# Optimization experiments

Measured on AMD Instinct MI355X. Metric: run time of the kernel, lower is better.

The kernel has to match this reference:

```python
import jax, jax.numpy as jnp
import numpy as np

ALPHA = 0.9          # alpha_mem
THRESHOLD = 1.0
WINDOW = 1.0         # module-level `window`; spike fn receives threshold*window
MEM_SUBTRACT = THRESHOLD  # membrane_subtract defaults to threshold


@jax.custom_vjp
def spike(v):
    # sinabs ThresholdSubtract forward: multiple spikes per step via floor division
    return jnp.where(v > 0, jnp.floor(v / THRESHOLD), 0.0)

def _spike_fwd(v):
    return spike(v), v

def _spike_bwd(v, g):
    # surrogate gradient: boxcar heaviside(v - (threshold - window)) / threshold
    grad = (v >= (THRESHOLD - THRESHOLD * WINDOW)).astype(g.dtype) / THRESHOLD
    return (g * grad,)

spike.defvjp(_spike_fwd, _spike_bwd)


def setup_inputs() -> dict:
    key = jax.random.key(0)
    k1, k2 = jax.random.split(key, 2)
    B, T, N = 32, 1000, 1024
    input_current = jax.random.normal(k1, (B, T, N), dtype=jnp.float32)
    w_rec = jax.random.normal(k2, (N, N), dtype=jnp.float32) * 0.02  # Linear weight [out, in]
    b_rec = jnp.zeros((N,), dtype=jnp.float32)
    return {"input_current": input_current, "w_rec": w_rec, "b_rec": b_rec}


def reference(input_current, w_rec, b_rec):
    B, T, N = input_current.shape

    def step(carry, x_t):
        state, rec = carry                      # [B, N] each
        total = x_t + rec                       # recurrent feedback added to input
        act = spike(state)                      # spikes from state BEFORE integration (1-step delay)
        state = state - act * MEM_SUBTRACT      # membrane subtract after spiking
        state = state * ALPHA + (1.0 - ALPHA) * total  # leaky integration
        rec = act @ w_rec.T + b_rec             # recurrent GEMM for next step
        return (state, rec), act

    state0 = jnp.zeros((B, N), dtype=input_current.dtype)
    rec0 = jnp.zeros((B, N), dtype=input_current.dtype)
    xs = jnp.swapaxes(input_current, 0, 1)      # [T, B, N]
    _, spikes = jax.lax.scan(step, (state0, rec0), xs)
    return jnp.swapaxes(spikes, 0, 1)           # [B, T, N]
```

## Files before the change

### kernel.cpp

```cpp
#include <hip/hip_runtime.h>
#include <cstdint>
#include <cstddef>

#define B_       32
#define T_       1000
#define N_       1024
#define THREADS_ 256
#define WAVES_   4
#define CHUNK_   8
#define NCHUNK_  (T_ / CHUNK_)

typedef float v4f __attribute__((ext_vector_type(4)));

__device__ __forceinline__ void barrier_lds() {
  __asm__ volatile("s_waitcnt lgkmcnt(0)\n\ts_barrier" ::: "memory");
}

#define ISSUE_CHUNK(buf, base)                                              \
  do {                                                                      \
    _Pragma("unroll")                                                       \
    for (int _k = 0; _k < CHUNK_; ++_k) {                                   \
      const v4f* _p = (const v4f*)((base) + (size_t)_k * N_);               \
      __asm__ volatile("global_load_dwordx4 %0, %1, off"                    \
                       : "=&v"(buf[_k])                                     \
                       : "v"(_p)                                            \
                       : "memory");                                         \
    }                                                                       \
  } while (0)

#define WAITBUF(buf, IMM)                                                   \
  __asm__ volatile("s_waitcnt vmcnt(" #IMM ")"                              \
                   : "+v"(buf[0]), "+v"(buf[1]), "+v"(buf[2]),              \
                     "+v"(buf[3]), "+v"(buf[4]), "+v"(buf[5]),              \
                     "+v"(buf[6]), "+v"(buf[7])                             \
                   :                                                        \
                   : "memory")

__global__ __launch_bounds__(THREADS_, 1)
void lif_main(const float* __restrict__ x, const float* __restrict__ w,
              const float* __restrict__ brec_g, float* __restrict__ out)
{
  const int b    = blockIdx.x;
  const int tid  = threadIdx.x;
  const int lane = tid & 63;
  const int wv   = tid >> 6;
  const int n0   = tid << 2;

  const float* xb   = x   + (size_t)b * T_ * N_ + n0;
  float*       outb = out + (size_t)b * T_ * N_ + n0;

  __shared__ unsigned long long s_cmask[2][WAVES_];
  __shared__ unsigned long long s_mask [2][WAVES_];
  __shared__ v4f                s_val  [2][THREADS_];

  v4f state = (v4f)(0.f);
  v4f rec   = (v4f)(0.f);
  const v4f brec = *(const v4f*)(brec_g + n0);

  auto process = [&](const v4f (&xs)[CHUNK_], int c) {
    v4f st = state;
    v4f r  = rec;
    v4f cmax = st;
#pragma unroll
    for (int k = 0; k < CHUNK_; ++k) {
      cmax.x = fmaxf(cmax.x, st.x);
      cmax.y = fmaxf(cmax.y, st.y);
      cmax.z = fmaxf(cmax.z, st.z);
      cmax.w = fmaxf(cmax.w, st.w);
      v4f t = xs[k] + r;
      st = st * 0.9f + 0.1f * t;
      r = brec;
    }
    float m = fmaxf(fmaxf(cmax.x, cmax.y), fmaxf(cmax.z, cmax.w));
    int any = (m >= 1.0f);

    const int p = c & 1;
    unsigned long long wm = __ballot(any);
    if (lane == 0) s_cmask[p][wv] = wm;
    barrier_lds();
    unsigned long long anyblk =
        s_cmask[p][0] | s_cmask[p][1] | s_cmask[p][2] | s_cmask[p][3];

    if (anyblk == 0ULL) {
      state = st;
      rec   = brec;
      return;
    }

    st = state;
    r  = rec;
#pragma unroll 1
    for (int k = 0; k < CHUNK_; ++k) {
      const int q = k & 1;
      float tx = xs[k].x + r.x, ty = xs[k].y + r.y,
            tz = xs[k].z + r.z, tw = xs[k].w + r.w;
      float ax = (st.x > 0.f) ? floorf(st.x) : 0.f;
      float ay = (st.y > 0.f) ? floorf(st.y) : 0.f;
      float az = (st.z > 0.f) ? floorf(st.z) : 0.f;
      float aw = (st.w > 0.f) ? floorf(st.w) : 0.f;
      int ms = (ax != 0.f) | (ay != 0.f) | (az != 0.f) | (aw != 0.f);
      if (ms) {
        v4f v; v.x = ax; v.y = ay; v.z = az; v.w = aw;
        s_val[q][tid] = v;
        size_t ot = (size_t)(c * CHUNK_ + k) * N_;
        if (ax != 0.f) outb[ot + 0] = ax;
        if (ay != 0.f) outb[ot + 1] = ay;
        if (az != 0.f) outb[ot + 2] = az;
        if (aw != 0.f) outb[ot + 3] = aw;
      }
      unsigned long long sm = __ballot(ms);
      if (lane == 0) s_mask[q][wv] = sm;
      st.x = (st.x - ax) * 0.9f + 0.1f * tx;
      st.y = (st.y - ay) * 0.9f + 0.1f * ty;
      st.z = (st.z - az) * 0.9f + 0.1f * tz;
      st.w = (st.w - aw) * 0.9f + 0.1f * tw;
      barrier_lds();
      v4f racc = brec;
#pragma unroll 1
      for (int w2 = 0; w2 < WAVES_; ++w2) {
        unsigned long long mm = s_mask[q][w2];
        while (mm) {
          int l = __builtin_ctzll(mm);
          mm &= mm - 1;
          int j = (w2 << 6) + l;
          v4f v = s_val[q][j];
          int jn = j << 2;
          if (v.x != 0.f) {
            racc.x += v.x * w[(size_t)(n0 + 0) * N_ + jn];
            racc.y += v.x * w[(size_t)(n0 + 1) * N_ + jn];
            racc.z += v.x * w[(size_t)(n0 + 2) * N_ + jn];
            racc.w += v.x * w[(size_t)(n0 + 3) * N_ + jn];
          }
          if (v.y != 0.f) {
            int j1 = jn + 1;
            racc.x += v.y * w[(size_t)(n0 + 0) * N_ + j1];
            racc.y += v.y * w[(size_t)(n0 + 1) * N_ + j1];
            racc.z += v.y * w[(size_t)(n0 + 2) * N_ + j1];
            racc.w += v.y * w[(size_t)(n0 + 3) * N_ + j1];
          }
          if (v.z != 0.f) {
            int j2 = jn + 2;
            racc.x += v.z * w[(size_t)(n0 + 0) * N_ + j2];
            racc.y += v.z * w[(size_t)(n0 + 1) * N_ + j2];
            racc.z += v.z * w[(size_t)(n0 + 2) * N_ + j2];
            racc.w += v.z * w[(size_t)(n0 + 3) * N_ + j2];
          }
          if (v.w != 0.f) {
            int j3 = jn + 3;
            racc.x += v.w * w[(size_t)(n0 + 0) * N_ + j3];
            racc.y += v.w * w[(size_t)(n0 + 1) * N_ + j3];
            racc.z += v.w * w[(size_t)(n0 + 2) * N_ + j3];
            racc.w += v.w * w[(size_t)(n0 + 3) * N_ + j3];
          }
        }
      }
      r = racc;
    }
    state = st;
    rec   = r;
  };

  v4f bufA[CHUNK_], bufB[CHUNK_], bufC[CHUNK_];
  ISSUE_CHUNK(bufA, xb);
  ISSUE_CHUNK(bufB, xb + (size_t)CHUNK_ * N_);

  int c = 0;
#pragma unroll 1
  for (int t3 = 0; t3 < 41; ++t3) {
    ISSUE_CHUNK(bufC, xb + (size_t)(c + 2) * CHUNK_ * N_);
    WAITBUF(bufA, 16);
    process(bufA, c); ++c;
    ISSUE_CHUNK(bufA, xb + (size_t)(c + 2) * CHUNK_ * N_);
    WAITBUF(bufB, 16);
    process(bufB, c); ++c;
    ISSUE_CHUNK(bufB, xb + (size_t)(c + 2) * CHUNK_ * N_);
    WAITBUF(bufC, 16);
    process(bufC, c); ++c;
  }
  WAITBUF(bufA, 8);
  process(bufA, 123);
  WAITBUF(bufB, 0);
  process(bufB, 124);
}

extern "C" void kernel_launch(void* const* d_in, const int* in_sizes, int n_in,
                              void* d_out, int out_size, void* d_ws, size_t ws_size,
                              hipStream_t stream) {
  const float* x  = (const float*)d_in[0];
  const float* w  = (const float*)d_in[1];
  const float* br = (const float*)d_in[2];
  float* out = (float*)d_out;

  hipMemsetAsync(out, 0, (size_t)out_size * sizeof(float), stream);

  lif_main<<<B_, THREADS_, 0, stream>>>(x, w, br, out);
}
```

Baseline: 351.4 us.

## Fuse output zeroing into main kernel, stage input via LDS, defer spike scatter

Replaces the separate memset with 2048 extra zeroing blocks launched alongside the 32 recurrent blocks, so clearing the output overlaps the serial time loop. Input chunks are now copied straight into shared memory with global_load_lds instead of into registers. Spikes are no longer written to the output inside the loop; they go into a per-batch workspace list through a shared atomic counter, and a second kernel scatters them afterwards so they cannot race with the zeroing. This relies on the spike count per batch staying under the capacity, otherwise spikes are silently dropped, and it adds a second kernel launch.

```diff
diff --git a/kernel.cpp b/kernel.cpp
--- a/kernel.cpp
+++ b/kernel.cpp
@@ -9,6 +9,7 @@
 #define WAVES_   4
 #define CHUNK_   8
 #define NCHUNK_  (T_ / CHUNK_)
+#define ZBLOCKS_ 2048
 
 typedef float v4f __attribute__((ext_vector_type(4)));
 
@@ -16,48 +17,65 @@
   __asm__ volatile("s_waitcnt lgkmcnt(0)\n\ts_barrier" ::: "memory");
 }
 
-#define ISSUE_CHUNK(buf, base)                                              \
-  do {                                                                      \
-    _Pragma("unroll")                                                       \
-    for (int _k = 0; _k < CHUNK_; ++_k) {                                   \
-      const v4f* _p = (const v4f*)((base) + (size_t)_k * N_);               \
-      __asm__ volatile("global_load_dwordx4 %0, %1, off"                    \
-                       : "=&v"(buf[_k])                                     \
-                       : "v"(_p)                                            \
-                       : "memory");                                         \
-    }                                                                       \
-  } while (0)
-
-#define WAITBUF(buf, IMM)                                                   \
-  __asm__ volatile("s_waitcnt vmcnt(" #IMM ")"                              \
-                   : "+v"(buf[0]), "+v"(buf[1]), "+v"(buf[2]),              \
-                     "+v"(buf[3]), "+v"(buf[4]), "+v"(buf[5]),              \
-                     "+v"(buf[6]), "+v"(buf[7])                             \
-                   :                                                        \
-                   : "memory")
+#define VMWAIT(N) __asm__ volatile("s_waitcnt vmcnt(" #N ")" ::: "memory")
+
+typedef const __attribute__((address_space(1))) void* gas_ptr;
+typedef __attribute__((address_space(3))) void*       las_ptr;
 
 __global__ __launch_bounds__(THREADS_, 1)
-void lif_main(const float* __restrict__ x, const float* __restrict__ w,
-              const float* __restrict__ brec_g, float* __restrict__ out)
+void lif_fused(const float* __restrict__ x, const float* __restrict__ w,
+               const float* __restrict__ brec_g, float* __restrict__ out,
+               unsigned long long* __restrict__ ws_rec,
+               unsigned int* __restrict__ ws_cnt, int cap)
 {
+  if (blockIdx.x >= B_) {
+    const size_t n4 = (size_t)B_ * T_ * N_ / 4;
+    size_t i = (size_t)(blockIdx.x - B_) * THREADS_ + threadIdx.x;
+    const size_t stride = (size_t)(gridDim.x - B_) * THREADS_;
+    v4f* o4 = (v4f*)out;
+    v4f z = (v4f)(0.f);
+    for (; i < n4; i += stride) __builtin_nontemporal_store(z, &o4[i]);
+    return;
+  }
+
   const int b    = blockIdx.x;
   const int tid  = threadIdx.x;
   const int lane = tid & 63;
   const int wv   = tid >> 6;
   const int n0   = tid << 2;
 
-  const float* xb   = x   + (size_t)b * T_ * N_ + n0;
-  float*       outb = out + (size_t)b * T_ * N_ + n0;
-
+  __shared__ float xbuf0[CHUNK_][N_];
+  __shared__ float xbuf1[CHUNK_][N_];
+  __shared__ float xbuf2[CHUNK_][N_];
   __shared__ unsigned long long s_cmask[2][WAVES_];
   __shared__ unsigned long long s_mask [2][WAVES_];
   __shared__ v4f                s_val  [2][THREADS_];
+  __shared__ unsigned int       s_spkcnt;
+
+  if (tid == 0) s_spkcnt = 0;
+
+  const float* xg = x + (size_t)b * T_ * N_ + (wv << 8) + (lane << 2);
 
   v4f state = (v4f)(0.f);
   v4f rec   = (v4f)(0.f);
   const v4f brec = *(const v4f*)(brec_g + n0);
 
-  auto process = [&](const v4f (&xs)[CHUNK_], int c) {
+#define ISSUE_LDS(bufv, c)                                                   \
+  do {                                                                       \
+    const float* _g = xg + (size_t)(c) * (CHUNK_ * N_);                      \
+    _Pragma("unroll")                                                        \
+    for (int _k = 0; _k < CHUNK_; ++_k)                                      \
+      __builtin_amdgcn_global_load_lds((gas_ptr)(_g + (size_t)_k * N_),      \
+                                       (las_ptr)&bufv[_k][wv << 8],          \
+                                       16, 0, 0);                            \
+  } while (0)
+
+  auto process = [&](const float* xrow, int c) {
+    v4f xs[CHUNK_];
+#pragma unroll
+    for (int k = 0; k < CHUNK_; ++k)
+      xs[k] = *(const v4f*)(xrow + (size_t)k * N_ + n0);
+
     v4f st = state;
     v4f r  = rec;
     v4f cmax = st;
@@ -102,11 +120,18 @@
       if (ms) {
         v4f v; v.x = ax; v.y = ay; v.z = az; v.w = aw;
         s_val[q][tid] = v;
-        size_t ot = (size_t)(c * CHUNK_ + k) * N_;
-        if (ax != 0.f) outb[ot + 0] = ax;
-        if (ay != 0.f) outb[ot + 1] = ay;
-        if (az != 0.f) outb[ot + 2] = az;
-        if (aw != 0.f) outb[ot + 3] = aw;
+        unsigned int off = (unsigned int)((c * CHUNK_ + k) * N_ + n0);
+        float av[4] = {ax, ay, az, aw};
+#pragma unroll
+        for (int e = 0; e < 4; ++e) {
+          if (av[e] != 0.f) {
+            unsigned int idx = atomicAdd(&s_spkcnt, 1u);
+            if ((int)idx < cap)
+              ws_rec[(size_t)b * cap + idx] =
+                  ((unsigned long long)(off + e) << 32) |
+                  (unsigned long long)__float_as_uint(av[e]);
+          }
+        }
       }
       unsigned long long sm = __ballot(ms);
       if (lane == 0) s_mask[q][wv] = sm;
@@ -160,27 +185,50 @@
     rec   = r;
   };
 
-  v4f bufA[CHUNK_], bufB[CHUNK_], bufC[CHUNK_];
-  ISSUE_CHUNK(bufA, xb);
-  ISSUE_CHUNK(bufB, xb + (size_t)CHUNK_ * N_);
+  const float* x0row = &xbuf0[0][0];
+  const float* x1row = &xbuf1[0][0];
+  const float* x2row = &xbuf2[0][0];
+
+  ISSUE_LDS(xbuf0, 0);
+  ISSUE_LDS(xbuf1, 1);
 
   int c = 0;
 #pragma unroll 1
   for (int t3 = 0; t3 < 41; ++t3) {
-    ISSUE_CHUNK(bufC, xb + (size_t)(c + 2) * CHUNK_ * N_);
-    WAITBUF(bufA, 16);
-    process(bufA, c); ++c;
-    ISSUE_CHUNK(bufA, xb + (size_t)(c + 2) * CHUNK_ * N_);
-    WAITBUF(bufB, 16);
-    process(bufB, c); ++c;
-    ISSUE_CHUNK(bufB, xb + (size_t)(c + 2) * CHUNK_ * N_);
-    WAITBUF(bufC, 16);
-    process(bufC, c); ++c;
+    ISSUE_LDS(xbuf2, c + 2);
+    VMWAIT(16);
+    process(x0row, c);
+    ISSUE_LDS(xbuf0, c + 3);
+    VMWAIT(16);
+    process(x1row, c + 1);
+    ISSUE_LDS(xbuf1, c + 4);
+    VMWAIT(16);
+    process(x2row, c + 2);
+    c += 3;
   }
-  WAITBUF(bufA, 8);
-  process(bufA, 123);
-  WAITBUF(bufB, 0);
-  process(bufB, 124);
+  VMWAIT(8);
+  process(x0row, 123);
+  VMWAIT(0);
+  process(x1row, 124);
+
+  __syncthreads();
+  if (tid == 0) ws_cnt[b] = s_spkcnt;
+#undef ISSUE_LDS
+}
+
+__global__ void scatter_spikes(const unsigned long long* __restrict__ rec,
+                               const unsigned int* __restrict__ cnt,
+                               float* __restrict__ out, int cap)
+{
+  int b = blockIdx.x;
+  unsigned int n = cnt[b];
+  if ((int)n > cap) n = cap;
+  for (unsigned int i = threadIdx.x; i < n; i += blockDim.x) {
+    unsigned long long r = rec[(size_t)b * cap + i];
+    unsigned int off = (unsigned int)(r >> 32);
+    float v = __uint_as_float((unsigned int)r);
+    out[(size_t)b * (T_ * N_) + off] = v;
+  }
 }
 
 extern "C" void kernel_launch(void* const* d_in, const int* in_sizes, int n_in,
@@ -191,7 +239,13 @@
   const float* br = (const float*)d_in[2];
   float* out = (float*)d_out;
 
-  hipMemsetAsync(out, 0, (size_t)out_size * sizeof(float), stream);
-
-  lif_main<<<B_, THREADS_, 0, stream>>>(x, w, br, out);
-}
+  int cap = 4096;
+  size_t need = (size_t)B_ * cap * 8 + B_ * 4;
+  if (ws_size < need && ws_size > 256)
+    cap = (int)((ws_size - 256) / ((size_t)B_ * 8));
+  unsigned long long* rec = (unsigned long long*)d_ws;
+  unsigned int* cnt = (unsigned int*)((char*)d_ws + (size_t)B_ * cap * 8);
+
+  lif_fused<<<B_ + ZBLOCKS_, THREADS_, 0, stream>>>(x, w, br, out, rec, cnt, cap);
+  scatter_spikes<<<B_, THREADS_, 0, stream>>>(rec, cnt, out, cap);
+}
```

Result: no change. 358.1 us (+1.9%).
